# Optimization experiments

Hardware: AMD Instinct MI355X
Metric: run time of the kernel (lower is better)

Reference implementation:

```python
import jax, jax.numpy as jnp
import numpy as np

D_MODEL = 768
NUM_HEADS = 12
HEAD_DIM = D_MODEL // NUM_HEADS
LN_EPS = 1e-5
MASK_NEG = -1000000.0


def setup_inputs() -> dict:
    key = jax.random.key(0)
    ks = jax.random.split(key, 10)
    B, L, S = 2, 2048, 2048
    s = 1.0 / np.sqrt(D_MODEL)
    return {
        "q": jax.random.normal(ks[0], (B, L, D_MODEL), jnp.float32),
        "k": jax.random.normal(ks[1], (B, S, D_MODEL), jnp.float32),
        "v": jax.random.normal(ks[2], (B, S, D_MODEL), jnp.float32),
        "attention_mask": jnp.ones((B, S), jnp.int32),
        "Wq": jax.random.normal(ks[3], (D_MODEL, D_MODEL), jnp.float32) * s,
        "Wk": jax.random.normal(ks[4], (D_MODEL, D_MODEL), jnp.float32) * s,
        "Wv": jax.random.normal(ks[5], (D_MODEL, D_MODEL), jnp.float32) * s,
        "W": jax.random.normal(ks[6], (D_MODEL, D_MODEL), jnp.float32) * s,
        "b": jnp.zeros((D_MODEL,), jnp.float32),
        "gamma": jnp.ones((D_MODEL,), jnp.float32),
        "beta": jnp.zeros((D_MODEL,), jnp.float32),
    }


def reference(q, k, v, attention_mask, Wq, Wk, Wv, W, b, gamma, beta):
    B, L, D = q.shape
    S = k.shape[1]
    H, hd = NUM_HEADS, HEAD_DIM
    # projections (torch Linear: x @ W^T), split heads -> (B,H,L,hd)
    Q = (q @ Wq.T).reshape(B, L, H, hd).transpose(0, 2, 1, 3)
    K = (k @ Wk.T).reshape(B, S, H, hd).transpose(0, 2, 1, 3)
    V = (v @ Wv.T).reshape(B, S, H, hd).transpose(0, 2, 1, 3)
    # scores (B,H,L,S) with additive key-padding mask
    scores = jnp.einsum("bhld,bhsd->bhls", Q, K) / np.sqrt(hd)
    mask_score = (1.0 - attention_mask.astype(q.dtype))[:, None, None, :] * MASK_NEG
    att = jax.nn.softmax(scores + mask_score, axis=-1)  # dropout p=0 (eval)
    # attend, merge heads, output projection (with bias)
    O = jnp.einsum("bhls,bhsd->bhld", att, V).transpose(0, 2, 1, 3).reshape(B, L, D)
    O = O @ W.T + b  # state dropout p=0 (eval)
    # residual + LayerNorm
    x = q + O
    mu = jnp.mean(x, axis=-1, keepdims=True)
    var = jnp.mean(jnp.square(x - mu), axis=-1, keepdims=True)
    return (x - mu) * jax.lax.rsqrt(var + LN_EPS) * gamma + beta
```

## Files before the change

### kernel.cpp

```cpp
#include <hip/hip_runtime.h>
#include <hip/hip_bf16.h>
#include <math.h>


typedef unsigned short u16;
typedef unsigned int   u32;
typedef __bf16 bf16x8 __attribute__((ext_vector_type(8)));
typedef float  f32x4  __attribute__((ext_vector_type(4)));

#define DM   768
#define MR   4096
#define WSZ  589824

#define LOG2E 1.44269504089f
#define SM_C  15.0f
#define K1    (0.125f * LOG2E)

__device__ inline u16 bfbits(float f) {
    union { __bf16 b; u16 u; } x; x.b = (__bf16)f; return x.u;
}

__device__ inline uint4 cvt8(const float* src) {
    const float4* p = reinterpret_cast<const float4*>(src);
    float4 a = p[0], b = p[1];
    union { __bf16 h[8]; uint4 v; } u;
    u.h[0] = (__bf16)a.x; u.h[1] = (__bf16)a.y; u.h[2] = (__bf16)a.z; u.h[3] = (__bf16)a.w;
    u.h[4] = (__bf16)b.x; u.h[5] = (__bf16)b.y; u.h[6] = (__bf16)b.z; u.h[7] = (__bf16)b.w;
    return u.v;
}

__device__ inline uint4 cvt8v(float4 a, float4 b) {
    union { __bf16 h[8]; uint4 v; } u;
    u.h[0] = (__bf16)a.x; u.h[1] = (__bf16)a.y; u.h[2] = (__bf16)a.z; u.h[3] = (__bf16)a.w;
    u.h[4] = (__bf16)b.x; u.h[5] = (__bf16)b.y; u.h[6] = (__bf16)b.z; u.h[7] = (__bf16)b.w;
    return u.v;
}

__global__ __launch_bounds__(256) void wcvt(
    const float* __restrict__ w0, const float* __restrict__ w1,
    const float* __restrict__ w2, const float* __restrict__ w3,
    u16* __restrict__ dst)
{
    const float* src = (blockIdx.y == 0) ? w0 : (blockIdx.y == 1) ? w1
                     : (blockIdx.y == 2) ? w2 : w3;
    size_t idx = ((size_t)blockIdx.x * 256 + threadIdx.x) * 8;
    *reinterpret_cast<uint4*>(&dst[(size_t)blockIdx.y * WSZ + idx]) = cvt8(&src[idx]);
}

__global__ __launch_bounds__(256, 2) void gemm_qkv(
    const float* __restrict__ xq, const float* __restrict__ xk, const float* __restrict__ xv,
    const u16* __restrict__ Wb4,
    u16* __restrict__ oq, u16* __restrict__ ok, u16* __restrict__ ov)
{
    const int mode = blockIdx.z;
    const float* X = (mode == 0) ? xq : (mode == 1) ? xk : xv;
    const u16* Wb  = Wb4 + (size_t)mode * WSZ;
    u16* out       = (mode == 0) ? oq : (mode == 1) ? ok : ov;

    __shared__ __attribute__((aligned(16))) u16 As[2][128][72];
    __shared__ __attribute__((aligned(16))) u16 Bs[2][128][72];

    const int tid  = threadIdx.x;
    const int lane = tid & 63;
    const int w    = tid >> 6;
    const int wm   = (w >> 1) * 64;
    const int wn   = (w & 1) * 64;
    const int quad = lane >> 4;
    const int l16  = lane & 15;
    const int tm   = blockIdx.x * 128;
    const int tn   = blockIdx.y * 128;

    const int srow = tid >> 1;
    const int scb  = (tid & 1) * 32;

    const float* aptr = &X[(size_t)(tm + srow) * 768 + scb];
    const u16*   bptr = &Wb[(size_t)(tn + srow) * 768 + scb];

    f32x4 acc[4][4] = {};

    {
        float4 at[8]; uint4 bt[4];
        #pragma unroll
        for (int i = 0; i < 8; i++)
            at[i] = *reinterpret_cast<const float4*>(aptr + i * 4);
        #pragma unroll
        for (int i = 0; i < 4; i++)
            bt[i] = *reinterpret_cast<const uint4*>(bptr + i * 8);
        #pragma unroll
        for (int i = 0; i < 4; i++) {
            *reinterpret_cast<uint4*>(&As[0][srow][scb + i * 8]) = cvt8v(at[2*i], at[2*i+1]);
            *reinterpret_cast<uint4*>(&Bs[0][srow][scb + i * 8]) = bt[i];
        }
    }

    for (int kt = 0; kt < 12; kt++) {
        const int cur = kt & 1;
        __syncthreads();

        float4 at[8]; uint4 bt[4];
        if (kt < 11) {
            const float* ap = aptr + (kt + 1) * 64;
            const u16*   bp = bptr + (kt + 1) * 64;
            #pragma unroll
            for (int i = 0; i < 8; i++)
                at[i] = *reinterpret_cast<const float4*>(ap + i * 4);
            #pragma unroll
            for (int i = 0; i < 4; i++)
                bt[i] = *reinterpret_cast<const uint4*>(bp + i * 8);
        }

        #pragma unroll
        for (int kk = 0; kk < 2; kk++) {
            bf16x8 af[4], bfr[4];
            #pragma unroll
            for (int i = 0; i < 4; i++)
                af[i] = *reinterpret_cast<const bf16x8*>(&As[cur][wm + i * 16 + l16][kk * 32 + quad * 8]);
            #pragma unroll
            for (int j = 0; j < 4; j++)
                bfr[j] = *reinterpret_cast<const bf16x8*>(&Bs[cur][wn + j * 16 + l16][kk * 32 + quad * 8]);
            #pragma unroll
            for (int i = 0; i < 4; i++)
                #pragma unroll
                for (int j = 0; j < 4; j++)
                    acc[i][j] = __builtin_amdgcn_mfma_f32_16x16x32_bf16(af[i], bfr[j], acc[i][j], 0, 0, 0);
        }

        if (kt < 11) {
            const int nxt = cur ^ 1;
            #pragma unroll
            for (int i = 0; i < 4; i++) {
                *reinterpret_cast<uint4*>(&As[nxt][srow][scb + i * 8]) = cvt8v(at[2*i], at[2*i+1]);
                *reinterpret_cast<uint4*>(&Bs[nxt][srow][scb + i * 8]) = bt[i];
            }
        }
    }

    #pragma unroll
    for (int i = 0; i < 4; i++)
        #pragma unroll
        for (int j = 0; j < 4; j++)
            #pragma unroll
            for (int r = 0; r < 4; r++) {
                int gm = tm + wm + i * 16 + quad * 4 + r;
                int gn = tn + wn + j * 16 + l16;
                int b = gm >> 11, l = gm & 2047;
                int h = gn >> 6,  d = gn & 63;
                u16 bv = bfbits(acc[i][j][r]);
                if (mode == 2)
                    out[((size_t)(b * 12 + h) * 64 + d) * 2048 + l] = bv;
                else
                    out[((size_t)(b * 12 + h) * 2048 + l) * 64 + d] = bv;
            }
}

__global__ __launch_bounds__(256) void gemm_out(
    const u16* __restrict__ Oa, const u16* __restrict__ Wb,
    const float* __restrict__ bias, const float* __restrict__ resid,
    float* __restrict__ Xb)
{
    __shared__ __attribute__((aligned(16))) u16 As[64][72];
    __shared__ __attribute__((aligned(16))) u16 Bs[64][72];

    const int tid  = threadIdx.x;
    const int lane = tid & 63;
    const int w    = tid >> 6;
    const int wm   = (w >> 1) * 32;
    const int wn   = (w & 1) * 32;
    const int quad = lane >> 4;
    const int l16  = lane & 15;
    const int tm   = blockIdx.x * 64;
    const int tn   = blockIdx.y * 64;

    f32x4 acc[2][2] = {};

    for (int k0 = 0; k0 < 768; k0 += 64) {
        __syncthreads();
        #pragma unroll
        for (int rep = 0; rep < 2; rep++) {
            int idx = tid + rep * 256;
            int row = idx >> 3;
            int col = (idx & 7) * 8;
            *reinterpret_cast<uint4*>(&As[row][col]) =
                *reinterpret_cast<const uint4*>(&Oa[(size_t)(tm + row) * 768 + k0 + col]);
            *reinterpret_cast<uint4*>(&Bs[row][col]) =
                *reinterpret_cast<const uint4*>(&Wb[(size_t)(tn + row) * 768 + k0 + col]);
        }
        __syncthreads();
        #pragma unroll
        for (int kk = 0; kk < 2; kk++) {
            bf16x8 a0 = *reinterpret_cast<const bf16x8*>(&As[wm + l16     ][kk*32 + quad*8]);
            bf16x8 a1 = *reinterpret_cast<const bf16x8*>(&As[wm + 16 + l16][kk*32 + quad*8]);
            bf16x8 b0 = *reinterpret_cast<const bf16x8*>(&Bs[wn + l16     ][kk*32 + quad*8]);
            bf16x8 b1 = *reinterpret_cast<const bf16x8*>(&Bs[wn + 16 + l16][kk*32 + quad*8]);
            acc[0][0] = __builtin_amdgcn_mfma_f32_16x16x32_bf16(a0, b0, acc[0][0], 0, 0, 0);
            acc[0][1] = __builtin_amdgcn_mfma_f32_16x16x32_bf16(a0, b1, acc[0][1], 0, 0, 0);
            acc[1][0] = __builtin_amdgcn_mfma_f32_16x16x32_bf16(a1, b0, acc[1][0], 0, 0, 0);
            acc[1][1] = __builtin_amdgcn_mfma_f32_16x16x32_bf16(a1, b1, acc[1][1], 0, 0, 0);
        }
    }

    #pragma unroll
    for (int i = 0; i < 2; i++)
        #pragma unroll
        for (int j = 0; j < 2; j++)
            #pragma unroll
            for (int r = 0; r < 4; r++) {
                int gm = tm + wm + i * 16 + quad * 4 + r;
                int gn = tn + wn + j * 16 + l16;
                Xb[(size_t)gm * 768 + gn] = acc[i][j][r] + bias[gn] + resid[(size_t)gm * 768 + gn];
            }
}

__global__ __launch_bounds__(256, 3) void attn(
    const u16* __restrict__ Qp, const u16* __restrict__ Kp, const u16* __restrict__ Vt,
    const int* __restrict__ amask, u16* __restrict__ Oatt)
{
    __shared__ __attribute__((aligned(16))) unsigned char smem[4 * 64 * 40 * 2 + 2048 * 4];
    u16 (*Ps)[64][40] = reinterpret_cast<u16(*)[64][40]>(smem);
    float* maskC = reinterpret_cast<float*>(smem + 20480);
    float (*Obuf)[72] = reinterpret_cast<float(*)[72]>(smem);

    const int tid  = threadIdx.x;
    const int lane = tid & 63;
    const int w    = tid >> 6;
    const int quad = lane >> 4;
    const int l16  = lane & 15;
    const int qt = blockIdx.x;
    const int h  = blockIdx.y;
    const int b  = blockIdx.z;

    #pragma unroll
    for (int i = 0; i < 8; i++) {
        int s = tid + i * 256;
        maskC[s] = amask[b * 2048 + s] ? (-SM_C * LOG2E) : -2.0e6f;
    }
    __syncthreads();

    const u16* Qbase = Qp + ((size_t)(b * 12 + h) * 2048 + qt * 64) * 64;
    const u16* Kb2   = Kp + (size_t)(b * 12 + h) * 2048 * 64 + (size_t)w * 32 * 64;
    const u16* Vb2   = Vt + (size_t)(b * 12 + h) * 64 * 2048 + (size_t)w * 32;

    bf16x8 qfrag[4][2];
    #pragma unroll
    for (int qb = 0; qb < 4; qb++)
        #pragma unroll
        for (int kk = 0; kk < 2; kk++)
            qfrag[qb][kk] = *reinterpret_cast<const bf16x8*>(
                &Qbase[(qb * 16 + l16) * 64 + kk * 32 + quad * 8]);

    bf16x8 onesf = {};
    if (l16 == 0) {
        #pragma unroll
        for (int i = 0; i < 8; i++) onesf[i] = (__bf16)1.0f;
    }

    f32x4 oacc[4][4] = {};
    f32x4 sacc[4]    = {};

    for (int st = 0; st < 16; st++) {
        bf16x8 kf[2][2], vf[4];
        #pragma unroll
        for (int ct = 0; ct < 2; ct++)
            #pragma unroll
            for (int kk = 0; kk < 2; kk++)
                kf[ct][kk] = *reinterpret_cast<const bf16x8*>(
                    &Kb2[(size_t)(st * 128 + ct * 16 + l16) * 64 + kk * 32 + quad * 8]);
        #pragma unroll
        for (int cd = 0; cd < 4; cd++)
            vf[cd] = *reinterpret_cast<const bf16x8*>(
                &Vb2[(size_t)(cd * 16 + l16) * 2048 + st * 128 + quad * 8]);

        float cc0 = maskC[st * 128 + w * 32 + l16];
        float cc1 = maskC[st * 128 + w * 32 + 16 + l16];

        #pragma unroll
        for (int qb = 0; qb < 4; qb++)
            #pragma unroll
            for (int ct = 0; ct < 2; ct++) {
                f32x4 s = {};
                s = __builtin_amdgcn_mfma_f32_16x16x32_bf16(qfrag[qb][0], kf[ct][0], s, 0, 0, 0);
                s = __builtin_amdgcn_mfma_f32_16x16x32_bf16(qfrag[qb][1], kf[ct][1], s, 0, 0, 0);
                float cc = ct ? cc1 : cc0;
                #pragma unroll
                for (int r = 0; r < 4; r++) {
                    float p = __builtin_amdgcn_exp2f(__builtin_fmaf(s[r], K1, cc));
                    Ps[w][qb * 16 + quad * 4 + r][ct * 16 + l16] = bfbits(p);
                }
            }

        bf16x8 pf[4];
        #pragma unroll
        for (int qb = 0; qb < 4; qb++)
            pf[qb] = *reinterpret_cast<const bf16x8*>(&Ps[w][qb * 16 + l16][quad * 8]);
        #pragma unroll
        for (int qb = 0; qb < 4; qb++)
            sacc[qb] = __builtin_amdgcn_mfma_f32_16x16x32_bf16(pf[qb], onesf, sacc[qb], 0, 0, 0);
        #pragma unroll
        for (int qb = 0; qb < 4; qb++)
            #pragma unroll
            for (int cd = 0; cd < 4; cd++)
                oacc[qb][cd] = __builtin_amdgcn_mfma_f32_16x16x32_bf16(pf[qb], vf[cd], oacc[qb][cd], 0, 0, 0);
    }

    __syncthreads();
    for (int wv = 0; wv < 4; wv++) {
        if (w == wv) {
            #pragma unroll
            for (int qb = 0; qb < 4; qb++) {
                #pragma unroll
                for (int cd = 0; cd < 4; cd++)
                    #pragma unroll
                    for (int r = 0; r < 4; r++) {
                        float* cell = &Obuf[qb * 16 + quad * 4 + r][cd * 16 + l16];
                        if (wv == 0) *cell = oacc[qb][cd][r];
                        else         *cell += oacc[qb][cd][r];
                    }
                if (l16 == 0) {
                    #pragma unroll
                    for (int r = 0; r < 4; r++) {
                        float* cell = &Obuf[qb * 16 + quad * 4 + r][64];
                        if (wv == 0) *cell = sacc[qb][r];
                        else         *cell += sacc[qb][r];
                    }
                }
            }
        }
        __syncthreads();
    }

    #pragma unroll
    for (int g = 0; g < 4; g++) {
        int unit = tid + g * 256;
        int row = unit >> 4;
        int c4  = (unit & 15) * 4;
        float rinv = 1.0f / Obuf[row][64];
        union { u16 h[4]; uint2 v; } o;
        #pragma unroll
        for (int j = 0; j < 4; j++)
            o.h[j] = bfbits(Obuf[row][c4 + j] * rinv);
        *reinterpret_cast<uint2*>(
            &Oatt[(size_t)(b * 2048 + qt * 64 + row) * 768 + h * 64 + c4]) = o.v;
    }
}

__global__ __launch_bounds__(256) void ln_kernel(
    float* __restrict__ X, const float* __restrict__ gamma,
    const float* __restrict__ beta)
{
    const int row = blockIdx.x;
    const int tid = threadIdx.x;
    float* xr = X + (size_t)row * 768;

    float v[3], s = 0.f, s2 = 0.f;
    #pragma unroll
    for (int i = 0; i < 3; i++) {
        v[i] = xr[tid + i * 256];
        s += v[i];
        s2 += v[i] * v[i];
    }
    #pragma unroll
    for (int off = 32; off >= 1; off >>= 1) {
        s  += __shfl_xor(s,  off, 64);
        s2 += __shfl_xor(s2, off, 64);
    }
    __shared__ float rs[4], rs2[4];
    int w = tid >> 6, lane = tid & 63;
    if (lane == 0) { rs[w] = s; rs2[w] = s2; }
    __syncthreads();
    s  = rs[0] + rs[1] + rs[2] + rs[3];
    s2 = rs2[0] + rs2[1] + rs2[2] + rs2[3];
    float mu = s * (1.0f / 768.0f);
    float var = s2 * (1.0f / 768.0f) - mu * mu;
    float rstd = rsqrtf(var + 1e-5f);
    #pragma unroll
    for (int i = 0; i < 3; i++) {
        int c = tid + i * 256;
        xr[c] = (v[i] - mu) * rstd * gamma[c] + beta[c];
    }
}

extern "C" void kernel_launch(void* const* d_in, const int* in_sizes, int n_in,
                              void* d_out, int out_size, void* d_ws, size_t ws_size,
                              hipStream_t stream)
{
    const float* q   = (const float*)d_in[0];
    const float* k   = (const float*)d_in[1];
    const float* v   = (const float*)d_in[2];
    const int*   am  = (const int*)d_in[3];
    const float* Wq  = (const float*)d_in[4];
    const float* Wk  = (const float*)d_in[5];
    const float* Wv  = (const float*)d_in[6];
    const float* W   = (const float*)d_in[7];
    const float* bb  = (const float*)d_in[8];
    const float* gam = (const float*)d_in[9];
    const float* bet = (const float*)d_in[10];

    u16* Wb4 = (u16*)d_ws;
    u16* Qp  = Wb4 + (size_t)4 * WSZ;
    u16* Kp  = Qp + (size_t)MR * DM;
    u16* Vt  = Kp + (size_t)MR * DM;
    u16* Oa  = Vt + (size_t)MR * DM;
    float* Xb = (float*)d_out;

    wcvt<<<dim3(288, 4), 256, 0, stream>>>(Wq, Wk, Wv, W, Wb4);
    gemm_qkv<<<dim3(32, 6, 3), 256, 0, stream>>>(q, k, v, Wb4, Qp, Kp, Vt);
    attn<<<dim3(32, 12, 2), 256, 0, stream>>>(Qp, Kp, Vt, am, Oa);
    gemm_out<<<dim3(64, 12), 256, 0, stream>>>(Oa, Wb4 + (size_t)3 * WSZ, bb, q, Xb);
    ln_kernel<<<4096, 256, 0, stream>>>(Xb, gam, bet);
}
```

Measured before the change: 247.4 us.

## Read QKV weight fragments from global directly and transpose score MFMA for packed P stores

The QKV projection GEMM drops the shared-memory staging buffer for the bf16 weight tile and loads each wave's B fragments straight from global memory inside the k-loop. This halves LDS use and removes the matching stores, but it exposes global-load latency in the MFMA loop with no prefetch, and it makes the two waves sharing a column block reload the same weights. In attention, the score MFMA operands are swapped so each lane holds four consecutive keys. The mask constants can then be read as one vector and the probabilities written to shared memory as a single packed 64-bit store instead of scattered 16-bit stores.

New measurement: 252.3 us. 2.0% more time.

```diff
diff --git a/kernel.cpp b/kernel.cpp
--- a/kernel.cpp
+++ b/kernel.cpp
@@ -58,7 +58,6 @@
     u16* out       = (mode == 0) ? oq : (mode == 1) ? ok : ov;
 
     __shared__ __attribute__((aligned(16))) u16 As[2][128][72];
-    __shared__ __attribute__((aligned(16))) u16 Bs[2][128][72];
 
     const int tid  = threadIdx.x;
     const int lane = tid & 63;
@@ -74,39 +73,34 @@
     const int scb  = (tid & 1) * 32;
 
     const float* aptr = &X[(size_t)(tm + srow) * 768 + scb];
-    const u16*   bptr = &Wb[(size_t)(tn + srow) * 768 + scb];
+    const u16* bbase = &Wb[(size_t)(tn + wn + l16) * 768];
 
     f32x4 acc[4][4] = {};
 
     {
-        float4 at[8]; uint4 bt[4];
+        float4 at[8];
         #pragma unroll
         for (int i = 0; i < 8; i++)
             at[i] = *reinterpret_cast<const float4*>(aptr + i * 4);
         #pragma unroll
         for (int i = 0; i < 4; i++)
-            bt[i] = *reinterpret_cast<const uint4*>(bptr + i * 8);
-        #pragma unroll
-        for (int i = 0; i < 4; i++) {
             *reinterpret_cast<uint4*>(&As[0][srow][scb + i * 8]) = cvt8v(at[2*i], at[2*i+1]);
-            *reinterpret_cast<uint4*>(&Bs[0][srow][scb + i * 8]) = bt[i];
-        }
     }
 
     for (int kt = 0; kt < 12; kt++) {
         const int cur = kt & 1;
         __syncthreads();
 
-        float4 at[8]; uint4 bt[4];
+        uint4 nw[4];
         if (kt < 11) {
             const float* ap = aptr + (kt + 1) * 64;
-            const u16*   bp = bptr + (kt + 1) * 64;
+            float4 at[8];
             #pragma unroll
             for (int i = 0; i < 8; i++)
                 at[i] = *reinterpret_cast<const float4*>(ap + i * 4);
             #pragma unroll
             for (int i = 0; i < 4; i++)
-                bt[i] = *reinterpret_cast<const uint4*>(bp + i * 8);
+                nw[i] = cvt8v(at[2*i], at[2*i+1]);
         }
 
         #pragma unroll
@@ -117,7 +111,8 @@
                 af[i] = *reinterpret_cast<const bf16x8*>(&As[cur][wm + i * 16 + l16][kk * 32 + quad * 8]);
             #pragma unroll
             for (int j = 0; j < 4; j++)
-                bfr[j] = *reinterpret_cast<const bf16x8*>(&Bs[cur][wn + j * 16 + l16][kk * 32 + quad * 8]);
+                bfr[j] = *reinterpret_cast<const bf16x8*>(
+                    &bbase[(size_t)j * 16 * 768 + kt * 64 + kk * 32 + quad * 8]);
             #pragma unroll
             for (int i = 0; i < 4; i++)
                 #pragma unroll
@@ -128,10 +123,8 @@
         if (kt < 11) {
             const int nxt = cur ^ 1;
             #pragma unroll
-            for (int i = 0; i < 4; i++) {
-                *reinterpret_cast<uint4*>(&As[nxt][srow][scb + i * 8]) = cvt8v(at[2*i], at[2*i+1]);
-                *reinterpret_cast<uint4*>(&Bs[nxt][srow][scb + i * 8]) = bt[i];
-            }
+            for (int i = 0; i < 4; i++)
+                *reinterpret_cast<uint4*>(&As[nxt][srow][scb + i * 8]) = nw[i];
         }
     }
 
@@ -270,22 +263,20 @@
             vf[cd] = *reinterpret_cast<const bf16x8*>(
                 &Vb2[(size_t)(cd * 16 + l16) * 2048 + st * 128 + quad * 8]);
 
-        float cc0 = maskC[st * 128 + w * 32 + l16];
-        float cc1 = maskC[st * 128 + w * 32 + 16 + l16];
-
         #pragma unroll
         for (int qb = 0; qb < 4; qb++)
             #pragma unroll
             for (int ct = 0; ct < 2; ct++) {
                 f32x4 s = {};
-                s = __builtin_amdgcn_mfma_f32_16x16x32_bf16(qfrag[qb][0], kf[ct][0], s, 0, 0, 0);
-                s = __builtin_amdgcn_mfma_f32_16x16x32_bf16(qfrag[qb][1], kf[ct][1], s, 0, 0, 0);
-                float cc = ct ? cc1 : cc0;
+                s = __builtin_amdgcn_mfma_f32_16x16x32_bf16(kf[ct][0], qfrag[qb][0], s, 0, 0, 0);
+                s = __builtin_amdgcn_mfma_f32_16x16x32_bf16(kf[ct][1], qfrag[qb][1], s, 0, 0, 0);
+                f32x4 cc = *reinterpret_cast<const f32x4*>(
+                    &maskC[st * 128 + w * 32 + ct * 16 + quad * 4]);
+                union { u16 h[4]; uint2 v2; } pk;
                 #pragma unroll
-                for (int r = 0; r < 4; r++) {
-                    float p = __builtin_amdgcn_exp2f(__builtin_fmaf(s[r], K1, cc));
-                    Ps[w][qb * 16 + quad * 4 + r][ct * 16 + l16] = bfbits(p);
-                }
+                for (int r = 0; r < 4; r++)
+                    pk.h[r] = bfbits(__builtin_amdgcn_exp2f(__builtin_fmaf(s[r], K1, cc[r])));
+                *reinterpret_cast<uint2*>(&Ps[w][qb * 16 + l16][ct * 16 + quad * 4]) = pk.v2;
             }
 
         bf16x8 pf[4];
```
